# Kernel optimization log

Hardware: AMD Instinct MI355X
Metric: run time of the kernel (lower is better)

The kernel has to match this reference:

```python
import jax, jax.numpy as jnp
import numpy as np

ALPHA = 0.7
NUM_HEADS = 12
NUM_KV_HEADS = 6
HEAD_DIM = 64
ROPE_BASE = 10000.0


def ternary_quantize(w):
    thr = ALPHA * jnp.mean(jnp.abs(w))
    return jnp.sign(w) * (jnp.abs(w) >= thr).astype(w.dtype)


def bitlinear(x, w):
    # forward: F.linear(x, ternary(w)) * mean(|w|)
    scale = jnp.mean(jnp.abs(w))
    qw = ternary_quantize(w)
    return (x @ qw.T) * scale


def rope_tables(seq_len, dim, dtype):
    inv_freq = 1.0 / (ROPE_BASE ** (jnp.arange(0, dim, 2, dtype=jnp.float32) / dim))
    t = jnp.arange(seq_len, dtype=jnp.float32)
    freqs = jnp.outer(t, inv_freq)            # [S, dim/2]
    emb = jnp.concatenate([freqs, freqs], -1)  # [S, dim]
    return jnp.cos(emb).astype(dtype), jnp.sin(emb).astype(dtype)


def rotate_half(x):
    x1, x2 = jnp.split(x, 2, axis=-1)
    return jnp.concatenate([-x2, x1], axis=-1)


def setup_inputs() -> dict:
    key = jax.random.key(0)
    ks = jax.random.split(key, 5)
    B, S, H = 2, 2048, 768
    return {
        "hidden_states": jax.random.normal(ks[0], (B, S, H), jnp.float32),
        "Wq": jax.random.normal(ks[1], (768, 768), jnp.float32) * 0.02,
        "Wk": jax.random.normal(ks[2], (384, 768), jnp.float32) * 0.02,
        "Wv": jax.random.normal(ks[3], (384, 768), jnp.float32) * 0.02,
        "Wo": jax.random.normal(ks[4], (768, 768), jnp.float32) * 0.02,
    }


def reference(hidden_states, Wq, Wk, Wv, Wo):
    B, S, H = hidden_states.shape
    nh, nkv, hd = NUM_HEADS, NUM_KV_HEADS, HEAD_DIM
    groups = nh // nkv

    q = bitlinear(hidden_states, Wq).reshape(B, S, nh, hd).transpose(0, 2, 1, 3)
    k = bitlinear(hidden_states, Wk).reshape(B, S, nkv, hd).transpose(0, 2, 1, 3)
    v = bitlinear(hidden_states, Wv).reshape(B, S, nkv, hd).transpose(0, 2, 1, 3)

    cos, sin = rope_tables(S, hd, hidden_states.dtype)  # [S, hd]
    cos = cos[None, None]  # [1,1,S,hd]
    sin = sin[None, None]
    q = q * cos + rotate_half(q) * sin
    k = k * cos + rotate_half(k) * sin

    # GQA: expand kv heads to full head count
    k = jnp.repeat(k, groups, axis=1)  # [B, nh, S, hd]
    v = jnp.repeat(v, groups, axis=1)

    scale = 1.0 / jnp.sqrt(jnp.asarray(hd, hidden_states.dtype))
    scores = jnp.einsum("bhsd,bhtd->bhst", q, k) * scale
    attn = jax.nn.softmax(scores, axis=-1)
    out = jnp.einsum("bhst,bhtd->bhsd", attn, v)
    out = out.transpose(0, 2, 1, 3).reshape(B, S, H)
    return bitlinear(out, Wo)
```

## Files before the change

kernel.cpp:

```cpp
#include <hip/hip_runtime.h>
#include <cmath>

typedef unsigned short u16;
typedef unsigned int u32;
typedef __bf16 bf16x2 __attribute__((ext_vector_type(2)));
typedef __bf16 bf16x8 __attribute__((ext_vector_type(8)));
typedef float f32x4 __attribute__((ext_vector_type(4)));
typedef float f32x16 __attribute__((ext_vector_type(16)));

#define NQ (768*768)
#define NK (384*768)

__device__ __forceinline__ u16 f2bf(float f) {
  u32 u = __float_as_uint(f);
  u32 r = (u + 0x7FFFu + ((u >> 16) & 1u)) >> 16;
  return (u16)r;
}
__device__ __forceinline__ u32 packbf(float a, float b) {
#if __has_builtin(__builtin_amdgcn_cvt_pk_bf16_f32)
  bf16x2 v = __builtin_amdgcn_cvt_pk_bf16_f32(a, b);
  u32 r; __builtin_memcpy(&r, &v, 4); return r;
#else
  return (u32)f2bf(a) | ((u32)f2bf(b) << 16);
#endif
}
__device__ __forceinline__ float fexp2(float x) {
#if __has_builtin(__builtin_amdgcn_exp2f)
  return __builtin_amdgcn_exp2f(x);
#else
  return exp2f(x);
#endif
}
__device__ __forceinline__ bf16x8 ldfrag(const u16* p) { bf16x8 v; __builtin_memcpy(&v, p, 16); return v; }
__device__ __forceinline__ f32x16 mfma32_(bf16x8 a, bf16x8 b, f32x16 c) {
  return __builtin_amdgcn_mfma_f32_32x32x16_bf16(a, b, c, 0, 0, 0);
}

__device__ __forceinline__ int kidx(int b6kvh, int s, int d) {
  return b6kvh * 131072 + (s >> 6) * 4096 + ((s >> 5) & 1) * 2048 + (d >> 4) * 512 +
         ((s & 31) + 32 * ((d >> 3) & 1)) * 8 + (d & 7);
}
__device__ __forceinline__ int qidx(int b, int s, int h, int d) {
  return ((b * 64 + (s >> 5)) * 12 + h) * 2048 + (d >> 4) * 512 +
         ((s & 31) + 32 * ((d >> 3) & 1)) * 8 + (d & 7);
}
__device__ __forceinline__ int vidx(int b6kvh, int d, int p) {
  return b6kvh * 131072 + (p >> 6) * 4096 + (d >> 5) * 2048 + ((p >> 4) & 3) * 512 +
         ((d & 31) + 32 * ((p >> 3) & 1)) * 8 + (p & 7);
}

__global__ __launch_bounds__(256) void abssum_kernel(const float* __restrict__ wq, const float* __restrict__ wk,
                                                     const float* __restrict__ wv, const float* __restrict__ wo,
                                                     float* __restrict__ sums) {
  int which = blockIdx.y;
  const float* w = (which == 0) ? wq : (which == 1) ? wk : (which == 2) ? wv : wo;
  int n4 = ((which == 0 || which == 3) ? NQ : NK) >> 2;
  const float4* w4 = (const float4*)w;
  float s = 0.f;
  for (int i = blockIdx.x * blockDim.x + threadIdx.x; i < n4; i += gridDim.x * blockDim.x) {
    float4 v = w4[i];
    s += fabsf(v.x) + fabsf(v.y) + fabsf(v.z) + fabsf(v.w);
  }
  for (int off = 32; off; off >>= 1) s += __shfl_down(s, off);
  __shared__ float ls[4];
  if ((threadIdx.x & 63) == 0) ls[threadIdx.x >> 6] = s;
  __syncthreads();
  if (threadIdx.x == 0) atomicAdd(&sums[which], ls[0] + ls[1] + ls[2] + ls[3]);
}

__global__ __launch_bounds__(256) void quant_kernel(const float* __restrict__ wq, const float* __restrict__ wk,
                                                    const float* __restrict__ wv, const float* __restrict__ wo,
                                                    const float* __restrict__ sums,
                                                    u16* __restrict__ qw, u16* __restrict__ woq) {
  float thr0 = 0.7f * sums[0] * (1.f / NQ);
  float thr1 = 0.7f * sums[1] * (1.f / NK);
  float thr2 = 0.7f * sums[2] * (1.f / NK);
  float thr3 = 0.7f * sums[3] * (1.f / NQ);
  const int NQKV = NQ + 2 * NK;
  const int total = NQKV + NQ;
  for (int i = blockIdx.x * blockDim.x + threadIdx.x; i < total; i += gridDim.x * blockDim.x) {
    float v, th; u16* dst;
    if (i < NQ)            { v = wq[i];            th = thr0; dst = &qw[i]; }
    else if (i < NQ + NK)  { v = wk[i - NQ];       th = thr1; dst = &qw[i]; }
    else if (i < NQKV)     { v = wv[i - NQ - NK];  th = thr2; dst = &qw[i]; }
    else                   { v = wo[i - NQKV];     th = thr3; dst = &woq[i - NQKV]; }
    float q = (fabsf(v) >= th) ? ((v > 0.f) ? 1.f : -1.f) : 0.f;
    *dst = f2bf(q);
  }
}

__global__ __launch_bounds__(256) void castx_kernel(const float* __restrict__ x, u16* __restrict__ xb) {
  int i = blockIdx.x * blockDim.x + threadIdx.x;
  float4 v = ((const float4*)x)[i];
  u16 o[4] = { f2bf(v.x), f2bf(v.y), f2bf(v.z), f2bf(v.w) };
  __builtin_memcpy(&xb[i * 4], o, 8);
}

__device__ __forceinline__ void gemm_tile_64x128(const u16* __restrict__ A, const u16* __restrict__ Bw,
                                                 u16* Bt, int tm, int tn, f32x16 acc[2]) {
  int t = threadIdx.x, lane = t & 63, w = t >> 6, c = lane & 31, g2 = lane >> 5;
  int wm = w & 1, wn = w >> 1;
  const u16* arow = A + (tm * 64 + wm * 32 + c) * 768;
  for (int k0 = 0; k0 < 768; k0 += 64) {
#pragma unroll
    for (int rd = 0; rd < 4; rd++) {
      int ch = (rd * 4 + w) * 64 + lane;
      int n = ch >> 3, jp = ch & 7;
      int jl = jp ^ (n & 7);
      const u16* gp = Bw + (tn * 128 + n) * 768 + k0 + jl * 8;
      __builtin_amdgcn_global_load_lds((const __attribute__((address_space(1))) u32*)gp,
                                       (__attribute__((address_space(3))) u32*)(Bt + (rd * 4 + w) * 512),
                                       16, 0, 0);
    }
    bf16x8 af[4];
#pragma unroll
    for (int ks = 0; ks < 4; ks++) af[ks] = ldfrag(arow + k0 + ks * 16 + g2 * 8);
    __syncthreads();
#pragma unroll
    for (int ks = 0; ks < 4; ks++) {
#pragma unroll
      for (int nb = 0; nb < 2; nb++) {
        int n = wn * 64 + nb * 32 + c;
        int jp = (ks * 2 + g2) ^ (n & 7);
        bf16x8 bf = ldfrag(Bt + n * 64 + jp * 8);
        acc[nb] = mfma32_(af[ks], bf, acc[nb]);
      }
    }
    __syncthreads();
  }
}

__global__ __launch_bounds__(256, 4) void gemm_qkv_kernel(const u16* __restrict__ xb, const u16* __restrict__ qw,
                                                          const float* __restrict__ sums,
                                                          u16* __restrict__ qb, u16* __restrict__ kb,
                                                          u16* __restrict__ vT) {
  __shared__ u16 Bt[8192];
  int tn = blockIdx.x, tm = blockIdx.y;
  f32x16 acc[2]; acc[0] = (f32x16)0.f; acc[1] = (f32x16)0.f;
  gemm_tile_64x128(xb, qw, Bt, tm, tn, acc);
  int t = threadIdx.x, lane = t & 63, w = t >> 6, c = lane & 31, g2 = lane >> 5;
  int wm = w & 1, wn = w >> 1;
  float sq = sums[0] * (1.f / NQ) * 0.180336880111120f;
  float sk = sums[1] * (1.f / NK);
  float sv = sums[2] * (1.f / NK);
  int mb = tm * 64 + wm * 32 + 4 * g2;
  if (tn < 9) {
    float sc = (tn < 6) ? sq : sk;
    int head = (tn < 6) ? (tn * 2 + wn) : ((tn - 6) * 2 + wn);
    float f = fexp2((float)c * -0.41524101186092029f);
#pragma unroll
    for (int r = 0; r < 16; r++) {
      int m = mb + (r & 3) + 8 * (r >> 2);
      int bb = m >> 11, s = m & 2047;
      float sn, cs; sincosf((float)s * f, &sn, &cs);
      float x1 = acc[0][r] * sc, x2 = acc[1][r] * sc;
      u16 y1 = f2bf(x1 * cs - x2 * sn);
      u16 y2 = f2bf(x2 * cs + x1 * sn);
      if (tn < 6) {
        qb[qidx(bb, s, head, c)]      = y1;
        qb[qidx(bb, s, head, c + 32)] = y2;
      } else {
        kb[kidx(bb * 6 + head, s, c)]      = y1;
        kb[kidx(bb * 6 + head, s, c + 32)] = y2;
      }
    }
  } else {
    int kvh = (tn - 9) * 2 + wn;
#pragma unroll
    for (int nb = 0; nb < 2; nb++)
#pragma unroll
      for (int r = 0; r < 16; r++) {
        int m = mb + (r & 3) + 8 * (r >> 2);
        int bb = m >> 11, s = m & 2047;
        int sp = (s & ~12) | ((s & 4) << 1) | ((s & 8) >> 1);
        vT[vidx(bb * 6 + kvh, nb * 32 + c, sp)] = f2bf(acc[nb][r] * sv);
      }
  }
}

__global__ __launch_bounds__(256, 2) void attn_kernel(const u16* __restrict__ qb, const u16* __restrict__ kb,
                                                      const u16* __restrict__ vT, u16* __restrict__ ab) {
  __shared__ float Obuf[4][32][66];
  __shared__ float Lbuf[2][4][32];
  int qt = blockIdx.x, bk = blockIdx.y;
  int b = bk / 6, kvh = bk % 6;
  int b6kvh = bk;
  int t = threadIdx.x, lane = t & 63, w = t >> 6, c = lane & 31, g2 = lane >> 5;

  bf16x8 qf[2][4];
#pragma unroll
  for (int qn = 0; qn < 2; qn++) {
    const u16* qbase = qb + ((b * 64 + qt) * 12 + (kvh * 2 + qn)) * 2048;
#pragma unroll
    for (int ks = 0; ks < 4; ks++)
      qf[qn][ks] = ldfrag(qbase + ks * 512 + lane * 8);
  }

  f32x16 fz = (f32x16)0.f;
  f32x16 O[2][2] = {{fz, fz}, {fz, fz}};
  float lsum[2] = {0.f, 0.f};

  const u16* kvbaseK = kb + b6kvh * 131072;
  const u16* kvbaseV = vT + b6kvh * 131072;

  for (int it = 0; it < 8; it++) {
    int kb64 = w * 8 + it;
    const u16* kt = kvbaseK + kb64 * 4096;
    const u16* vt = kvbaseV + kb64 * 4096;
    bf16x8 kf[2][4];
#pragma unroll
    for (int km = 0; km < 2; km++)
#pragma unroll
      for (int ks = 0; ks < 4; ks++)
        kf[km][ks] = ldfrag(kt + km * 2048 + ks * 512 + lane * 8);
    f32x16 S[2][2] = {{fz, fz}, {fz, fz}};
#pragma unroll
    for (int ks = 0; ks < 4; ks++)
#pragma unroll
      for (int km = 0; km < 2; km++)
#pragma unroll
        for (int qn = 0; qn < 2; qn++)
          S[km][qn] = mfma32_(kf[km][ks], qf[qn][ks], S[km][qn]);
    bf16x8 vf[2][4];
#pragma unroll
    for (int dn = 0; dn < 2; dn++)
#pragma unroll
      for (int ks = 0; ks < 4; ks++)
        vf[dn][ks] = ldfrag(vt + dn * 2048 + ks * 512 + lane * 8);
    bf16x8 PA[2][4];
#pragma unroll
    for (int qn = 0; qn < 2; qn++) {
#pragma unroll
      for (int km = 0; km < 2; km++) {
        float e[16];
#pragma unroll
        for (int r = 0; r < 16; r++) {
          e[r] = fexp2(S[km][qn][r]);
          lsum[qn] += e[r];
        }
        u32 P[8];
#pragma unroll
        for (int j = 0; j < 8; j++) P[j] = packbf(e[2 * j], e[2 * j + 1]);
        __builtin_memcpy(&PA[qn][km * 2 + 0], &P[0], 16);
        __builtin_memcpy(&PA[qn][km * 2 + 1], &P[4], 16);
      }
    }
#pragma unroll
    for (int ks = 0; ks < 4; ks++)
#pragma unroll
      for (int qn = 0; qn < 2; qn++)
#pragma unroll
        for (int dn = 0; dn < 2; dn++)
          O[qn][dn] = mfma32_(PA[qn][ks], vf[dn][ks], O[qn][dn]);
  }
#pragma unroll
  for (int qn = 0; qn < 2; qn++) lsum[qn] += __shfl_xor(lsum[qn], 32);
  if (g2 == 0) { Lbuf[0][w][c] = lsum[0]; Lbuf[1][w][c] = lsum[1]; }
#pragma unroll
  for (int qn = 0; qn < 2; qn++) {
    if (qn) __syncthreads();
#pragma unroll
    for (int dn = 0; dn < 2; dn++)
#pragma unroll
      for (int r = 0; r < 16; r++) {
        int qq = (r & 3) + 8 * (r >> 2) + 4 * g2;
        Obuf[w][qq][dn * 32 + c] = O[qn][dn][r];
      }
    __syncthreads();
    int qq = t >> 3, dc = (t & 7) * 8;
    float l = Lbuf[qn][0][qq] + Lbuf[qn][1][qq] + Lbuf[qn][2][qq] + Lbuf[qn][3][qq];
    float inv = 1.f / l;
    u16 o[8];
#pragma unroll
    for (int j = 0; j < 8; j++) {
      float s = Obuf[0][qq][dc + j] + Obuf[1][qq][dc + j] + Obuf[2][qq][dc + j] + Obuf[3][qq][dc + j];
      o[j] = f2bf(s * inv);
    }
    __builtin_memcpy(ab + (b * 2048 + qt * 32 + qq) * 768 + (kvh * 2 + qn) * 64 + dc, o, 16);
  }
}

__global__ __launch_bounds__(256, 4) void gemm_out_kernel(const u16* __restrict__ ab, const u16* __restrict__ woq,
                                                          const float* __restrict__ sums, float* __restrict__ out) {
  __shared__ u16 Bt[8192];
  int tn = blockIdx.x, tm = blockIdx.y;
  f32x16 acc[2]; acc[0] = (f32x16)0.f; acc[1] = (f32x16)0.f;
  gemm_tile_64x128(ab, woq, Bt, tm, tn, acc);
  int t = threadIdx.x, lane = t & 63, w = t >> 6, c = lane & 31, g2 = lane >> 5;
  int wm = w & 1, wn = w >> 1;
  float so = sums[3] * (1.f / NQ);
  int mb = tm * 64 + wm * 32 + 4 * g2;
#pragma unroll
  for (int nb = 0; nb < 2; nb++)
#pragma unroll
    for (int r = 0; r < 16; r++) {
      int m = mb + (r & 3) + 8 * (r >> 2);
      out[m * 768 + tn * 128 + wn * 64 + nb * 32 + c] = acc[nb][r] * so;
    }
}

extern "C" void kernel_launch(void* const* d_in, const int* in_sizes, int n_in,
                              void* d_out, int out_size, void* d_ws, size_t ws_size,
                              hipStream_t stream) {
  const float* x  = (const float*)d_in[0];
  const float* wq = (const float*)d_in[1];
  const float* wk = (const float*)d_in[2];
  const float* wv = (const float*)d_in[3];
  const float* wo = (const float*)d_in[4];
  float* out = (float*)d_out;
  char* ws = (char*)d_ws;

  float* sums = (float*)ws;
  u16* qw  = (u16*)(ws + 256);
  u16* woq = (u16*)(ws + 2359552);
  u16* xb  = (u16*)(ws + 3539200);
  u16* qb  = (u16*)(ws + 9830656);
  u16* kb  = (u16*)(ws + 16122112);
  u16* vT  = (u16*)(ws + 19267840);
  u16* ab  = (u16*)(ws + 22413568);

  hipMemsetAsync(sums, 0, 16, stream);
  dim3 blk(256);
  abssum_kernel<<<dim3(64, 4), blk, 0, stream>>>(wq, wk, wv, wo, sums);
  quant_kernel<<<dim3(6912), blk, 0, stream>>>(wq, wk, wv, wo, sums, qw, woq);
  castx_kernel<<<dim3(3072), blk, 0, stream>>>(x, xb);
  gemm_qkv_kernel<<<dim3(12, 64), blk, 0, stream>>>(xb, qw, sums, qb, kb, vT);
  attn_kernel<<<dim3(64, 12), blk, 0, stream>>>(qb, kb, vT, ab);
  gemm_out_kernel<<<dim3(6, 64), blk, 0, stream>>>(ab, woq, sums, out);
}
```

Before: 172.2 us.

## Pre-swizzle A operands into MFMA fragment layout and restructure attention warps

```diff
diff --git a/kernel.cpp b/kernel.cpp
--- a/kernel.cpp
+++ b/kernel.cpp
@@ -5,7 +5,6 @@
 typedef unsigned int u32;
 typedef __bf16 bf16x2 __attribute__((ext_vector_type(2)));
 typedef __bf16 bf16x8 __attribute__((ext_vector_type(8)));
-typedef float f32x4 __attribute__((ext_vector_type(4)));
 typedef float f32x16 __attribute__((ext_vector_type(16)));
 
 #define NQ (768*768)
@@ -37,7 +36,7 @@
 }
 
 __device__ __forceinline__ int kidx(int b6kvh, int s, int d) {
-  return b6kvh * 131072 + (s >> 6) * 4096 + ((s >> 5) & 1) * 2048 + (d >> 4) * 512 +
+  return b6kvh * 131072 + (s >> 5) * 2048 + (d >> 4) * 512 +
          ((s & 31) + 32 * ((d >> 3) & 1)) * 8 + (d & 7);
 }
 __device__ __forceinline__ int qidx(int b, int s, int h, int d) {
@@ -47,6 +46,9 @@
 __device__ __forceinline__ int vidx(int b6kvh, int d, int p) {
   return b6kvh * 131072 + (p >> 6) * 4096 + (d >> 5) * 2048 + ((p >> 4) & 3) * 512 +
          ((d & 31) + 32 * ((p >> 3) & 1)) * 8 + (p & 7);
+}
+__device__ __forceinline__ int fidx(int m, int k) {
+  return (m >> 5) * 24576 + (k >> 4) * 512 + ((m & 31) + 32 * ((k >> 3) & 1)) * 8 + (k & 7);
 }
 
 __global__ __launch_bounds__(256) void abssum_kernel(const float* __restrict__ wq, const float* __restrict__ wk,
@@ -90,17 +92,21 @@
 }
 
 __global__ __launch_bounds__(256) void castx_kernel(const float* __restrict__ x, u16* __restrict__ xb) {
-  int i = blockIdx.x * blockDim.x + threadIdx.x;
-  float4 v = ((const float4*)x)[i];
-  u16 o[4] = { f2bf(v.x), f2bf(v.y), f2bf(v.z), f2bf(v.w) };
-  __builtin_memcpy(&xb[i * 4], o, 8);
+  int idx = blockIdx.x * blockDim.x + threadIdx.x;
+  int m = idx / 96, k8 = idx - m * 96;
+  const float4* xp = (const float4*)(x + m * 768 + k8 * 8);
+  float4 v0 = xp[0], v1 = xp[1];
+  u16 o[8] = { f2bf(v0.x), f2bf(v0.y), f2bf(v0.z), f2bf(v0.w),
+               f2bf(v1.x), f2bf(v1.y), f2bf(v1.z), f2bf(v1.w) };
+  u16* dst = xb + (m >> 5) * 24576 + (k8 >> 1) * 512 + ((m & 31) + 32 * (k8 & 1)) * 8;
+  __builtin_memcpy(dst, o, 16);
 }
 
 __device__ __forceinline__ void gemm_tile_64x128(const u16* __restrict__ A, const u16* __restrict__ Bw,
                                                  u16* Bt, int tm, int tn, f32x16 acc[2]) {
   int t = threadIdx.x, lane = t & 63, w = t >> 6, c = lane & 31, g2 = lane >> 5;
   int wm = w & 1, wn = w >> 1;
-  const u16* arow = A + (tm * 64 + wm * 32 + c) * 768;
+  const u16* abase = A + (tm * 2 + wm) * 24576 + lane * 8;
   for (int k0 = 0; k0 < 768; k0 += 64) {
 #pragma unroll
     for (int rd = 0; rd < 4; rd++) {
@@ -114,7 +120,7 @@
     }
     bf16x8 af[4];
 #pragma unroll
-    for (int ks = 0; ks < 4; ks++) af[ks] = ldfrag(arow + k0 + ks * 16 + g2 * 8);
+    for (int ks = 0; ks < 4; ks++) af[ks] = ldfrag(abase + ((k0 >> 4) + ks) * 512);
     __syncthreads();
 #pragma unroll
     for (int ks = 0; ks < 4; ks++) {
@@ -178,125 +184,128 @@
   }
 }
 
-__global__ __launch_bounds__(256, 2) void attn_kernel(const u16* __restrict__ qb, const u16* __restrict__ kb,
+__global__ __launch_bounds__(256, 3) void attn_kernel(const u16* __restrict__ qb, const u16* __restrict__ kb,
                                                       const u16* __restrict__ vT, u16* __restrict__ ab) {
   __shared__ float Obuf[4][32][66];
-  __shared__ float Lbuf[2][4][32];
+  __shared__ float Lbuf[4][32];
   int qt = blockIdx.x, bk = blockIdx.y;
   int b = bk / 6, kvh = bk % 6;
-  int b6kvh = bk;
   int t = threadIdx.x, lane = t & 63, w = t >> 6, c = lane & 31, g2 = lane >> 5;
-
-  bf16x8 qf[2][4];
-#pragma unroll
-  for (int qn = 0; qn < 2; qn++) {
-    const u16* qbase = qb + ((b * 64 + qt) * 12 + (kvh * 2 + qn)) * 2048;
-#pragma unroll
-    for (int ks = 0; ks < 4; ks++)
-      qf[qn][ks] = ldfrag(qbase + ks * 512 + lane * 8);
-  }
+  int qn = w & 1, kh = w >> 1;
+
+  const u16* qbase = qb + ((b * 64 + qt) * 12 + kvh * 2 + qn) * 2048;
+  bf16x8 qf[4];
+#pragma unroll
+  for (int ks = 0; ks < 4; ks++) qf[ks] = ldfrag(qbase + ks * 512 + lane * 8);
+
+  u32 onesw = 0x3F803F80u;
+  bf16x8 ones;
+  { u32 tmp[4] = {onesw, onesw, onesw, onesw}; __builtin_memcpy(&ones, tmp, 16); }
 
   f32x16 fz = (f32x16)0.f;
-  f32x16 O[2][2] = {{fz, fz}, {fz, fz}};
-  float lsum[2] = {0.f, 0.f};
-
-  const u16* kvbaseK = kb + b6kvh * 131072;
-  const u16* kvbaseV = vT + b6kvh * 131072;
-
-  for (int it = 0; it < 8; it++) {
-    int kb64 = w * 8 + it;
-    const u16* kt = kvbaseK + kb64 * 4096;
-    const u16* vt = kvbaseV + kb64 * 4096;
-    bf16x8 kf[2][4];
-#pragma unroll
-    for (int km = 0; km < 2; km++)
-#pragma unroll
-      for (int ks = 0; ks < 4; ks++)
-        kf[km][ks] = ldfrag(kt + km * 2048 + ks * 512 + lane * 8);
-    f32x16 S[2][2] = {{fz, fz}, {fz, fz}};
-#pragma unroll
-    for (int ks = 0; ks < 4; ks++)
-#pragma unroll
-      for (int km = 0; km < 2; km++)
-#pragma unroll
-        for (int qn = 0; qn < 2; qn++)
-          S[km][qn] = mfma32_(kf[km][ks], qf[qn][ks], S[km][qn]);
-    bf16x8 vf[2][4];
+  f32x16 O[2] = {fz, fz};
+  f32x16 Lacc = fz;
+
+  const u16* Kb = kb + bk * 131072;
+  const u16* Vb = vT + bk * 131072;
+
+  for (int it = 0; it < 32; it++) {
+    int kb32 = kh * 32 + it;
+    const u16* kt = Kb + kb32 * 2048;
+    const u16* vt = Vb + (kb32 >> 1) * 4096 + (kb32 & 1) * 1024;
+    bf16x8 kf[4];
+#pragma unroll
+    for (int ks = 0; ks < 4; ks++) kf[ks] = ldfrag(kt + ks * 512 + lane * 8);
+    bf16x8 vf[2][2];
 #pragma unroll
     for (int dn = 0; dn < 2; dn++)
 #pragma unroll
-      for (int ks = 0; ks < 4; ks++)
-        vf[dn][ks] = ldfrag(vt + dn * 2048 + ks * 512 + lane * 8);
-    bf16x8 PA[2][4];
-#pragma unroll
-    for (int qn = 0; qn < 2; qn++) {
-#pragma unroll
-      for (int km = 0; km < 2; km++) {
-        float e[16];
-#pragma unroll
-        for (int r = 0; r < 16; r++) {
-          e[r] = fexp2(S[km][qn][r]);
-          lsum[qn] += e[r];
-        }
-        u32 P[8];
-#pragma unroll
-        for (int j = 0; j < 8; j++) P[j] = packbf(e[2 * j], e[2 * j + 1]);
-        __builtin_memcpy(&PA[qn][km * 2 + 0], &P[0], 16);
-        __builtin_memcpy(&PA[qn][km * 2 + 1], &P[4], 16);
-      }
-    }
-#pragma unroll
-    for (int ks = 0; ks < 4; ks++)
-#pragma unroll
-      for (int qn = 0; qn < 2; qn++)
-#pragma unroll
-        for (int dn = 0; dn < 2; dn++)
-          O[qn][dn] = mfma32_(PA[qn][ks], vf[dn][ks], O[qn][dn]);
-  }
-#pragma unroll
-  for (int qn = 0; qn < 2; qn++) lsum[qn] += __shfl_xor(lsum[qn], 32);
-  if (g2 == 0) { Lbuf[0][w][c] = lsum[0]; Lbuf[1][w][c] = lsum[1]; }
-#pragma unroll
-  for (int qn = 0; qn < 2; qn++) {
-    if (qn) __syncthreads();
-#pragma unroll
-    for (int dn = 0; dn < 2; dn++)
-#pragma unroll
-      for (int r = 0; r < 16; r++) {
-        int qq = (r & 3) + 8 * (r >> 2) + 4 * g2;
-        Obuf[w][qq][dn * 32 + c] = O[qn][dn][r];
-      }
-    __syncthreads();
-    int qq = t >> 3, dc = (t & 7) * 8;
-    float l = Lbuf[qn][0][qq] + Lbuf[qn][1][qq] + Lbuf[qn][2][qq] + Lbuf[qn][3][qq];
+      for (int ksv = 0; ksv < 2; ksv++)
+        vf[dn][ksv] = ldfrag(vt + dn * 2048 + ksv * 512 + lane * 8);
+    f32x16 S = fz;
+#pragma unroll
+    for (int ks = 0; ks < 4; ks++) S = mfma32_(kf[ks], qf[ks], S);
+    float e[16];
+#pragma unroll
+    for (int r = 0; r < 16; r++) e[r] = fexp2(S[r]);
+    u32 P[8];
+#pragma unroll
+    for (int j = 0; j < 8; j++) P[j] = packbf(e[2 * j], e[2 * j + 1]);
+    bf16x8 PA[2];
+    __builtin_memcpy(&PA[0], &P[0], 16);
+    __builtin_memcpy(&PA[1], &P[4], 16);
+#pragma unroll
+    for (int ksv = 0; ksv < 2; ksv++) {
+      O[0] = mfma32_(PA[ksv], vf[0][ksv], O[0]);
+      O[1] = mfma32_(PA[ksv], vf[1][ksv], O[1]);
+      Lacc = mfma32_(PA[ksv], ones, Lacc);
+    }
+  }
+  if (c == 0) {
+#pragma unroll
+    for (int r = 0; r < 16; r++) Lbuf[w][(r & 3) + 8 * (r >> 2) + 4 * g2] = Lacc[r];
+  }
+#pragma unroll
+  for (int dn = 0; dn < 2; dn++)
+#pragma unroll
+    for (int r = 0; r < 16; r++)
+      Obuf[w][(r & 3) + 8 * (r >> 2) + 4 * g2][dn * 32 + c] = O[dn][r];
+  __syncthreads();
+  {
+    int hn = t >> 7, qq = (t >> 2) & 31, dc = (t & 3) * 16;
+    float l = Lbuf[hn][qq] + Lbuf[hn + 2][qq];
     float inv = 1.f / l;
-    u16 o[8];
-#pragma unroll
-    for (int j = 0; j < 8; j++) {
-      float s = Obuf[0][qq][dc + j] + Obuf[1][qq][dc + j] + Obuf[2][qq][dc + j] + Obuf[3][qq][dc + j];
-      o[j] = f2bf(s * inv);
-    }
-    __builtin_memcpy(ab + (b * 2048 + qt * 32 + qq) * 768 + (kvh * 2 + qn) * 64 + dc, o, 16);
+    u16 o[16];
+#pragma unroll
+    for (int j = 0; j < 16; j++)
+      o[j] = f2bf((Obuf[hn][qq][dc + j] + Obuf[hn + 2][qq][dc + j]) * inv);
+    int h = kvh * 2 + hn;
+    int mg = b * 64 + qt;
+    u16* dst = ab + mg * 24576 + ((h * 64 + dc) >> 4) * 512 + qq * 8;
+    __builtin_memcpy(dst, o, 16);
+    __builtin_memcpy(dst + 256, o + 8, 16);
   }
 }
 
 __global__ __launch_bounds__(256, 4) void gemm_out_kernel(const u16* __restrict__ ab, const u16* __restrict__ woq,
                                                           const float* __restrict__ sums, float* __restrict__ out) {
-  __shared__ u16 Bt[8192];
+  __shared__ u16 Bt[4096];
   int tn = blockIdx.x, tm = blockIdx.y;
-  f32x16 acc[2]; acc[0] = (f32x16)0.f; acc[1] = (f32x16)0.f;
-  gemm_tile_64x128(ab, woq, Bt, tm, tn, acc);
   int t = threadIdx.x, lane = t & 63, w = t >> 6, c = lane & 31, g2 = lane >> 5;
   int wm = w & 1, wn = w >> 1;
+  f32x16 acc = (f32x16)0.f;
+  const u16* abase = ab + (tm * 2 + wm) * 24576 + lane * 8;
+  for (int k0 = 0; k0 < 768; k0 += 64) {
+#pragma unroll
+    for (int rd = 0; rd < 2; rd++) {
+      int ch = (rd * 4 + w) * 64 + lane;
+      int n = ch >> 3, jp = ch & 7;
+      int jl = jp ^ (n & 7);
+      const u16* gp = woq + (tn * 64 + n) * 768 + k0 + jl * 8;
+      __builtin_amdgcn_global_load_lds((const __attribute__((address_space(1))) u32*)gp,
+                                       (__attribute__((address_space(3))) u32*)(Bt + (rd * 4 + w) * 512),
+                                       16, 0, 0);
+    }
+    bf16x8 af[4];
+#pragma unroll
+    for (int ks = 0; ks < 4; ks++) af[ks] = ldfrag(abase + ((k0 >> 4) + ks) * 512);
+    __syncthreads();
+#pragma unroll
+    for (int ks = 0; ks < 4; ks++) {
+      int n = wn * 32 + c;
+      int jp = (ks * 2 + g2) ^ (n & 7);
+      bf16x8 bf = ldfrag(Bt + n * 64 + jp * 8);
+      acc = mfma32_(af[ks], bf, acc);
+    }
+    __syncthreads();
+  }
   float so = sums[3] * (1.f / NQ);
   int mb = tm * 64 + wm * 32 + 4 * g2;
 #pragma unroll
-  for (int nb = 0; nb < 2; nb++)
-#pragma unroll
-    for (int r = 0; r < 16; r++) {
-      int m = mb + (r & 3) + 8 * (r >> 2);
-      out[m * 768 + tn * 128 + wn * 64 + nb * 32 + c] = acc[nb][r] * so;
-    }
+  for (int r = 0; r < 16; r++) {
+    int m = mb + (r & 3) + 8 * (r >> 2);
+    out[m * 768 + tn * 64 + wn * 32 + c] = acc[r] * so;
+  }
 }
 
 extern "C" void kernel_launch(void* const* d_in, const int* in_sizes, int n_in,
@@ -323,8 +332,8 @@
   dim3 blk(256);
   abssum_kernel<<<dim3(64, 4), blk, 0, stream>>>(wq, wk, wv, wo, sums);
   quant_kernel<<<dim3(6912), blk, 0, stream>>>(wq, wk, wv, wo, sums, qw, woq);
-  castx_kernel<<<dim3(3072), blk, 0, stream>>>(x, xb);
+  castx_kernel<<<dim3(1536), blk, 0, stream>>>(x, xb);
   gemm_qkv_kernel<<<dim3(12, 64), blk, 0, stream>>>(xb, qw, sums, qb, kb, vT);
   attn_kernel<<<dim3(64, 12), blk, 0, stream>>>(qb, kb, vT, ab);
-  gemm_out_kernel<<<dim3(6, 64), blk, 0, stream>>>(ab, woq, sums, out);
-}
+  gemm_out_kernel<<<dim3(12, 64), blk, 0, stream>>>(ab, woq, sums, out);
+}
```

New measurement: 157.5 us. 1.09x faster.
